# Kernel tuning notes

Measured on AMD Instinct MI355X. Metric: run time of the kernel, lower is better.

## Reference

```python
import jax, jax.numpy as jnp
import numpy as np

N = 100000
E = 1600000
F_NODE = 6
F_EDGE = 2
H = 64


def _glorot(key, shape):
    lim = float(np.sqrt(6.0 / (shape[0] + shape[1])))
    return jax.random.uniform(key, shape, jnp.float32, -lim, lim)


def setup_inputs() -> dict:
    key = jax.random.key(0)
    ks = jax.random.split(key, 16)
    inp = {
        "x": jax.random.normal(ks[0], (N, F_NODE), jnp.float32),
        "edge_index": jax.random.randint(ks[1], (2, E), 0, N, jnp.int64),
        "edge_attr": jax.random.normal(ks[2], (E, F_EDGE), jnp.float32),
        # GCN layers (PyG GCNConv: linear no-bias, then aggregate, then +bias)
        "W1": _glorot(ks[3], (F_NODE, H)), "b1": jnp.zeros((H,), jnp.float32),
        "W2": _glorot(ks[4], (H, H)), "b2": jnp.zeros((H,), jnp.float32),
        "W3": _glorot(ks[5], (H, H)), "b3": jnp.zeros((H,), jnp.float32),
        # edge_mlp
        "We1": _glorot(ks[6], (F_EDGE, H)), "be1": jnp.zeros((H,), jnp.float32),
        "We2": _glorot(ks[7], (H, H)), "be2": jnp.zeros((H,), jnp.float32),
        # predictor
        "Wp1": _glorot(ks[8], (3 * H, H)), "bp1": jnp.zeros((H,), jnp.float32),
        "Wp2": _glorot(ks[9], (H, H // 2)), "bp2": jnp.zeros((H // 2,), jnp.float32),
        "Wp3": _glorot(ks[10], (H // 2, 1)), "bp3": jnp.zeros((1,), jnp.float32),
    }
    return inp


def _gcn_conv(h, W, b, src_sl, dst_sl, norm, n):
    # PyG GCNConv with self-loops and symmetric normalization
    h = h @ W                                   # [N, H_out]
    msg = h[src_sl] * norm[:, None]             # gather + scale per edge(+loop)
    out = jax.ops.segment_sum(msg, dst_sl, num_segments=n)
    return out + b


def _forward(x, edge_attr, W1, b1, W2, b2, W3, b3, We1, be1, We2, be2,
             Wp1, bp1, Wp2, bp2, Wp3, bp3, edge_index):
    n = x.shape[0]
    src, dst = edge_index[0], edge_index[1]

    # --- edge feature injection (vectorized version of per-edge loop) ---
    ef = jax.nn.relu(edge_attr @ We1 + be1) @ We2 + be2      # [E, H]
    nef = (jax.ops.segment_sum(ef, src, num_segments=n)
           + jax.ops.segment_sum(ef, dst, num_segments=n))   # [N, H]
    ones_e = jnp.ones((ef.shape[0],), x.dtype)
    deg = (jax.ops.segment_sum(ones_e, src, num_segments=n)
           + jax.ops.segment_sum(ones_e, dst, num_segments=n))
    deg = jnp.maximum(deg, 1.0)
    nef = nef / deg[:, None]
    # hidden_dim (64) >= node feature dim (6) -> truncate
    x = x + nef[:, : x.shape[1]] * 0.5

    # --- GCN normalization with self-loops (shared across layers) ---
    loop = jnp.arange(n, dtype=src.dtype)
    src_sl = jnp.concatenate([src, loop])
    dst_sl = jnp.concatenate([dst, loop])
    deg_sl = jax.ops.segment_sum(jnp.ones_like(dst_sl, dtype=x.dtype), dst_sl,
                                 num_segments=n)
    dinv = jnp.where(deg_sl > 0, deg_sl ** -0.5, 0.0)
    norm = dinv[src_sl] * dinv[dst_sl]

    h = jax.nn.relu(_gcn_conv(x, W1, b1, src_sl, dst_sl, norm, n))
    h = jax.nn.relu(_gcn_conv(h, W2, b2, src_sl, dst_sl, norm, n))
    h = _gcn_conv(h, W3, b3, src_sl, dst_sl, norm, n)

    graph_emb = h.mean(axis=0)                 # global_mean_pool, batch=None
    node_mean = h.mean(axis=0)
    node_std = jnp.std(h, axis=0, ddof=1)      # torch.std is unbiased
    combined = jnp.concatenate([graph_emb, node_mean, node_std])  # [3H]

    p = jax.nn.relu(combined @ Wp1 + bp1)      # dropout inactive in eval
    p = jax.nn.relu(p @ Wp2 + bp2)
    out = jax.nn.sigmoid(p @ Wp3 + bp3)        # (1,)
    return out


def reference(x, edge_index, edge_attr, W1, b1, W2, b2, W3, b3,
              We1, be1, We2, be2, Wp1, bp1, Wp2, bp2, Wp3, bp3):
    return _forward(x, edge_attr, W1, b1, W2, b2, W3, b3, We1, be1, We2, be2,
                    Wp1, bp1, Wp2, bp2, Wp3, bp3, edge_index)
```

## Files before the change

kernel.cpp:

```cpp
#include <hip/hip_runtime.h>
#include <hip/hip_bf16.h>
#include <stdint.h>

typedef float floatx2 __attribute__((ext_vector_type(2)));

__device__ __forceinline__ float rdlane(float v, int l) {
    return __uint_as_float(__builtin_amdgcn_readlane(__float_as_uint(v), l));
}
__device__ __forceinline__ float bf2f(unsigned short u) {
    return __uint_as_float(((unsigned)u) << 16);
}
__device__ __forceinline__ unsigned short f2bf(float f) {
    unsigned u = __float_as_uint(f);
    u += 0x7fffu + ((u >> 16) & 1u);
    return (unsigned short)(u >> 16);
}
__device__ __forceinline__ unsigned packbf(float a, float b) {
    return (unsigned)f2bf(a) | ((unsigned)f2bf(b) << 16);
}
__device__ __forceinline__ unsigned pk_fp8x4(float a, float b, float c, float d) {
    int u = __builtin_amdgcn_cvt_pk_fp8_f32(a, b, 0, false);
    u = __builtin_amdgcn_cvt_pk_fp8_f32(c, d, u, true);
    return (unsigned)u;
}

__global__ void k_zero(int* __restrict__ cntO, int* __restrict__ cntI,
                       double* __restrict__ sums, int n) {
    int i = blockIdx.x * blockDim.x + threadIdx.x;
    if (i < 128) sums[i] = 0.0;
    if (i < n) { cntO[i] = 0; cntI[i] = 0; }
}

__global__ __launch_bounds__(256) void k_front(
    const int* __restrict__ ei, const float* __restrict__ ea,
    const float* __restrict__ We1, const float* __restrict__ be1,
    const float* __restrict__ We2, const float* __restrict__ be2,
    unsigned* __restrict__ efp, int* __restrict__ cntO, int* __restrict__ cntI,
    int* __restrict__ rankS, int* __restrict__ rankD, int E) {
    __shared__ float sWe1[128], sbe1[64], sWe2[64 * 6], sbe2[6];
    int t = threadIdx.x;
    if (t < 128) sWe1[t] = We1[t];
    if (t < 64) {
        sbe1[t] = be1[t];
#pragma unroll
        for (int c = 0; c < 6; ++c) sWe2[t * 6 + c] = We2[t * 64 + c];
    }
    if (t < 6) sbe2[t] = be2[t];
    __syncthreads();

    int e = blockIdx.x * blockDim.x + t;
    if (e >= E) return;

    int s = ei[e], d = ei[E + e];
    int rs = atomicAdd(&cntO[s], 1);
    int rd = atomicAdd(&cntI[d], 1);

    float2 aa = ((const float2*)ea)[e];
    float a0 = aa.x, a1 = aa.y;
    float acc[6];
#pragma unroll
    for (int c = 0; c < 6; ++c) acc[c] = sbe2[c];
#pragma unroll
    for (int j = 0; j < 64; ++j) {
        float h = fmaf(a0, sWe1[j], fmaf(a1, sWe1[64 + j], sbe1[j]));
        h = fmaxf(h, 0.f);
#pragma unroll
        for (int c = 0; c < 6; ++c) acc[c] = fmaf(h, sWe2[j * 6 + c], acc[c]);
    }
    unsigned* q = efp + (size_t)e * 3;
    q[0] = packbf(acc[0], acc[1]);
    q[1] = packbf(acc[2], acc[3]);
    q[2] = packbf(acc[4], acc[5]);
    rankS[e] = rs;
    rankD[e] = rd;
}

__global__ __launch_bounds__(256) void k_scan1(const int* __restrict__ cntO,
                                               const int* __restrict__ cntI,
                                               int2* __restrict__ bsum, int n) {
    __shared__ int2 l[256];
    int i = blockIdx.x * 256 + threadIdx.x;
    l[threadIdx.x] = (i < n) ? make_int2(cntO[i], cntI[i]) : make_int2(0, 0);
    __syncthreads();
    for (int s = 128; s > 0; s >>= 1) {
        if (threadIdx.x < s) {
            l[threadIdx.x].x += l[threadIdx.x + s].x;
            l[threadIdx.x].y += l[threadIdx.x + s].y;
        }
        __syncthreads();
    }
    if (threadIdx.x == 0) bsum[blockIdx.x] = l[0];
}

__global__ __launch_bounds__(512) void k_scan2(int2* __restrict__ bsum, int nb,
                                               int* __restrict__ offON,
                                               int* __restrict__ offIN) {
    __shared__ int2 l[512];
    int t = threadIdx.x;
    int2 v = (t < nb) ? bsum[t] : make_int2(0, 0);
    l[t] = v;
    __syncthreads();
    for (int s = 1; s < 512; s <<= 1) {
        int2 tmp = (t >= s) ? l[t - s] : make_int2(0, 0);
        __syncthreads();
        l[t].x += tmp.x; l[t].y += tmp.y;
        __syncthreads();
    }
    if (t < nb) bsum[t] = make_int2(l[t].x - v.x, l[t].y - v.y);
    if (t == 511) { *offON = l[511].x; *offIN = l[511].y; }
}

__global__ __launch_bounds__(256) void k_scan3off(const int* __restrict__ cntO,
                                                  const int* __restrict__ cntI,
                                                  const int2* __restrict__ bsum,
                                                  int* __restrict__ offO,
                                                  int* __restrict__ offI, int n) {
    __shared__ int2 l[256];
    int i = blockIdx.x * 256 + threadIdx.x;
    int2 v = (i < n) ? make_int2(cntO[i], cntI[i]) : make_int2(0, 0);
    l[threadIdx.x] = v;
    __syncthreads();
    for (int s = 1; s < 256; s <<= 1) {
        int2 tmp = (threadIdx.x >= (unsigned)s) ? l[threadIdx.x - s] : make_int2(0, 0);
        __syncthreads();
        l[threadIdx.x].x += tmp.x; l[threadIdx.x].y += tmp.y;
        __syncthreads();
    }
    if (i < n) {
        int2 bs = bsum[blockIdx.x];
        offO[i] = l[threadIdx.x].x - v.x + bs.x;
        offI[i] = l[threadIdx.x].y - v.y + bs.y;
    }
}

__global__ __launch_bounds__(256) void k_place(const int* __restrict__ ei,
                                               const int* __restrict__ rankS,
                                               const int* __restrict__ rankD,
                                               const int* __restrict__ offO,
                                               const int* __restrict__ offI,
                                               const unsigned* __restrict__ efp,
                                               unsigned* __restrict__ out_rec,
                                               uint4* __restrict__ in_rec, int E) {
    int e = blockIdx.x * blockDim.x + threadIdx.x;
    if (e >= E) return;
    int s = ei[e], d = ei[E + e];
    const unsigned* q = efp + (size_t)e * 3;
    unsigned u0 = q[0], u1 = q[1], u2 = q[2];
    size_t so = (size_t)(offO[s] + rankS[e]) * 3;
    out_rec[so] = u0; out_rec[so + 1] = u1; out_rec[so + 2] = u2;
    in_rec[offI[d] + rankD[e]] = make_uint4((unsigned)s, u0, u1, u2);
}

__global__ __launch_bounds__(256) void k_nef_x(
    const int* __restrict__ offO, const unsigned* __restrict__ out_rec,
    const int* __restrict__ offI, const uint4* __restrict__ in_rec,
    const float* __restrict__ x,
    float* __restrict__ xp, float* __restrict__ dinv, int n) {
    int i = blockIdx.x * blockDim.x + threadIdx.x;
    if (i >= n) return;
    int bo = offO[i], eo = offO[i + 1];
    int bi = offI[i], eiN = offI[i + 1];
    float a0 = 0.f, a1 = 0.f, a2 = 0.f, a3 = 0.f, a4 = 0.f, a5 = 0.f;
    for (int j = bo; j < eo; ++j) {
        const unsigned* q = out_rec + (size_t)j * 3;
        unsigned u0 = q[0], u1 = q[1], u2 = q[2];
        a0 += bf2f((unsigned short)u0); a1 += bf2f((unsigned short)(u0 >> 16));
        a2 += bf2f((unsigned short)u1); a3 += bf2f((unsigned short)(u1 >> 16));
        a4 += bf2f((unsigned short)u2); a5 += bf2f((unsigned short)(u2 >> 16));
    }
    for (int j = bi; j < eiN; ++j) {
        uint4 r = in_rec[j];
        a0 += bf2f((unsigned short)r.y); a1 += bf2f((unsigned short)(r.y >> 16));
        a2 += bf2f((unsigned short)r.z); a3 += bf2f((unsigned short)(r.z >> 16));
        a4 += bf2f((unsigned short)r.w); a5 += bf2f((unsigned short)(r.w >> 16));
    }
    int indeg = eiN - bi;
    float degf = (float)((eo - bo) + indeg);
    float inv = 0.5f / fmaxf(degf, 1.f);
    xp[(size_t)i * 6 + 0] = x[(size_t)i * 6 + 0] + a0 * inv;
    xp[(size_t)i * 6 + 1] = x[(size_t)i * 6 + 1] + a1 * inv;
    xp[(size_t)i * 6 + 2] = x[(size_t)i * 6 + 2] + a2 * inv;
    xp[(size_t)i * 6 + 3] = x[(size_t)i * 6 + 3] + a3 * inv;
    xp[(size_t)i * 6 + 4] = x[(size_t)i * 6 + 4] + a4 * inv;
    xp[(size_t)i * 6 + 5] = x[(size_t)i * 6 + 5] + a5 * inv;
    dinv[i] = 1.f / sqrtf(1.f + (float)indeg);
}

__global__ __launch_bounds__(256) void k_mm1(const float* __restrict__ xp,
                                             const float* __restrict__ W1,
                                             const float* __restrict__ dinv,
                                             unsigned* __restrict__ sOut, int n) {
    int lane = threadIdx.x & 63;
    int sub = lane & 15;
    int wid = (blockIdx.x * blockDim.x + threadIdx.x) >> 6;
    int nw = (gridDim.x * blockDim.x) >> 6;
    float w[6];
#pragma unroll
    for (int c = 0; c < 6; ++c) w[c] = W1[c * 64 + lane];
    for (int i = wid; i < n; i += nw) {
        float xv = (lane < 6) ? xp[(size_t)i * 6 + lane] : 0.f;
        float acc = 0.f;
#pragma unroll
        for (int c = 0; c < 6; ++c) acc = fmaf(rdlane(xv, c), w[c], acc);
        float o = acc * dinv[i];
        float o0 = __shfl(o, sub * 4 + 0);
        float o1 = __shfl(o, sub * 4 + 1);
        float o2 = __shfl(o, sub * 4 + 2);
        float o3 = __shfl(o, sub * 4 + 3);
        if (lane < 16) sOut[(size_t)i * 16 + lane] = pk_fp8x4(o0, o1, o2, o3);
    }
}

__global__ __launch_bounds__(256) void k_gathermm(
    const int* __restrict__ offI, const uint4* __restrict__ in_rec,
    const float* __restrict__ dinv, const unsigned* __restrict__ sIn,
    const float* __restrict__ bias, const float* __restrict__ W,
    unsigned* __restrict__ sOut, int n) {
    int lane = threadIdx.x & 63;
    int sub = lane & 15, grp = lane >> 4;
    int wid = (blockIdx.x * blockDim.x + threadIdx.x) >> 6;
    int nw = (gridDim.x * blockDim.x) >> 6;
    float w[64];
#pragma unroll
    for (int c = 0; c < 64; ++c) w[c] = W[c * 64 + lane];
    float4 bb = ((const float4*)bias)[sub];

    for (int i = wid; i < n; i += nw) {
        unsigned su = sIn[(size_t)i * 16 + sub];
        float a0, a1, a2, a3;
        if (grp == 0) {
            floatx2 lo = __builtin_amdgcn_cvt_pk_f32_fp8(su, false);
            floatx2 hi = __builtin_amdgcn_cvt_pk_f32_fp8(su, true);
            a0 = lo.x; a1 = lo.y; a2 = hi.x; a3 = hi.y;
        } else { a0 = a1 = a2 = a3 = 0.f; }
        int b0 = offI[i], e0 = offI[i + 1];
#pragma unroll 4
        for (int j = b0 + grp; j < e0; j += 4) {
            unsigned src = in_rec[j].x;
            unsigned u = sIn[(size_t)src * 16 + sub];
            floatx2 lo = __builtin_amdgcn_cvt_pk_f32_fp8(u, false);
            floatx2 hi = __builtin_amdgcn_cvt_pk_f32_fp8(u, true);
            a0 += lo.x; a1 += lo.y; a2 += hi.x; a3 += hi.y;
        }
        a0 += __shfl_xor(a0, 16); a1 += __shfl_xor(a1, 16);
        a2 += __shfl_xor(a2, 16); a3 += __shfl_xor(a3, 16);
        a0 += __shfl_xor(a0, 32); a1 += __shfl_xor(a1, 32);
        a2 += __shfl_xor(a2, 32); a3 += __shfl_xor(a3, 32);

        float dv = dinv[i];
        float h0 = fmaxf(fmaf(a0, dv, bb.x), 0.f);
        float h1 = fmaxf(fmaf(a1, dv, bb.y), 0.f);
        float h2 = fmaxf(fmaf(a2, dv, bb.z), 0.f);
        float h3 = fmaxf(fmaf(a3, dv, bb.w), 0.f);
        float o = 0.f;
#pragma unroll
        for (int g = 0; g < 16; ++g) {
            o = fmaf(rdlane(h0, g), w[g * 4 + 0], o);
            o = fmaf(rdlane(h1, g), w[g * 4 + 1], o);
            o = fmaf(rdlane(h2, g), w[g * 4 + 2], o);
            o = fmaf(rdlane(h3, g), w[g * 4 + 3], o);
        }
        o *= dv;
        float o0 = __shfl(o, sub * 4 + 0);
        float o1 = __shfl(o, sub * 4 + 1);
        float o2 = __shfl(o, sub * 4 + 2);
        float o3 = __shfl(o, sub * 4 + 3);
        if (lane < 16) sOut[(size_t)i * 16 + lane] = pk_fp8x4(o0, o1, o2, o3);
    }
}

__global__ __launch_bounds__(256) void k_gatherreduce(
    const int* __restrict__ offI, const uint4* __restrict__ in_rec,
    const float* __restrict__ dinv, const unsigned* __restrict__ sIn,
    const float* __restrict__ b3, double* __restrict__ sums, int n) {
    int lane = threadIdx.x & 63;
    int sub = lane & 15, grp = lane >> 4;
    int wv = threadIdx.x >> 6;
    int wid = (blockIdx.x * blockDim.x + threadIdx.x) >> 6;
    int nw = (gridDim.x * blockDim.x) >> 6;
    float4 bb = ((const float4*)b3)[sub];
    double s0 = 0.0, s1 = 0.0, s2_ = 0.0, s3 = 0.0;
    double q0 = 0.0, q1 = 0.0, q2 = 0.0, q3 = 0.0;

    for (int i = wid; i < n; i += nw) {
        unsigned su = sIn[(size_t)i * 16 + sub];
        float a0, a1, a2, a3;
        if (grp == 0) {
            floatx2 lo = __builtin_amdgcn_cvt_pk_f32_fp8(su, false);
            floatx2 hi = __builtin_amdgcn_cvt_pk_f32_fp8(su, true);
            a0 = lo.x; a1 = lo.y; a2 = hi.x; a3 = hi.y;
        } else { a0 = a1 = a2 = a3 = 0.f; }
        int b0 = offI[i], e0 = offI[i + 1];
#pragma unroll 4
        for (int j = b0 + grp; j < e0; j += 4) {
            unsigned src = in_rec[j].x;
            unsigned u = sIn[(size_t)src * 16 + sub];
            floatx2 lo = __builtin_amdgcn_cvt_pk_f32_fp8(u, false);
            floatx2 hi = __builtin_amdgcn_cvt_pk_f32_fp8(u, true);
            a0 += lo.x; a1 += lo.y; a2 += hi.x; a3 += hi.y;
        }
        a0 += __shfl_xor(a0, 16); a1 += __shfl_xor(a1, 16);
        a2 += __shfl_xor(a2, 16); a3 += __shfl_xor(a3, 16);
        a0 += __shfl_xor(a0, 32); a1 += __shfl_xor(a1, 32);
        a2 += __shfl_xor(a2, 32); a3 += __shfl_xor(a3, 32);

        float dv = dinv[i];
        float v0 = fmaf(a0, dv, bb.x);
        float v1 = fmaf(a1, dv, bb.y);
        float v2 = fmaf(a2, dv, bb.z);
        float v3 = fmaf(a3, dv, bb.w);
        s0 += v0; s1 += v1; s2_ += v2; s3 += v3;
        q0 += (double)v0 * v0; q1 += (double)v1 * v1;
        q2 += (double)v2 * v2; q3 += (double)v3 * v3;
    }
    __shared__ double shS[4 * 64], shQ[4 * 64];
    if (grp == 0) {
#pragma unroll
        for (int k = 0; k < 4; ++k) {
            double sk = (k == 0) ? s0 : (k == 1) ? s1 : (k == 2) ? s2_ : s3;
            double qk = (k == 0) ? q0 : (k == 1) ? q1 : (k == 2) ? q2 : q3;
            shS[wv * 64 + sub * 4 + k] = sk;
            shQ[wv * 64 + sub * 4 + k] = qk;
        }
    }
    __syncthreads();
    if (wv == 0) {
        double a = shS[lane] + shS[64 + lane] + shS[128 + lane] + shS[192 + lane];
        double c = shQ[lane] + shQ[64 + lane] + shQ[128 + lane] + shQ[192 + lane];
        unsafeAtomicAdd(&sums[lane], a);
        unsafeAtomicAdd(&sums[64 + lane], c);
    }
}

__global__ void k_head(const double* __restrict__ sums,
                       const float* __restrict__ Wp1, const float* __restrict__ bp1,
                       const float* __restrict__ Wp2, const float* __restrict__ bp2,
                       const float* __restrict__ Wp3, const float* __restrict__ bp3,
                       float* __restrict__ out, int n) {
    __shared__ float comb[192], p1[64], p2[32];
    int t = threadIdx.x;
    if (t < 64) {
        double s = sums[t], s2 = sums[64 + t];
        double m = s / n;
        double var = (s2 - s * s / n) / (double)(n - 1);
        float mf = (float)m;
        float sd = (float)sqrt(var > 0.0 ? var : 0.0);
        comb[t] = mf;
        comb[64 + t] = mf;
        comb[128 + t] = sd;
    }
    __syncthreads();
    if (t < 64) {
        float acc = bp1[t];
        for (int k = 0; k < 192; ++k) acc = fmaf(comb[k], Wp1[k * 64 + t], acc);
        p1[t] = fmaxf(acc, 0.f);
    }
    __syncthreads();
    if (t < 32) {
        float acc = bp2[t];
        for (int k = 0; k < 64; ++k) acc = fmaf(p1[k], Wp2[k * 32 + t], acc);
        p2[t] = fmaxf(acc, 0.f);
    }
    __syncthreads();
    if (t == 0) {
        float acc = bp3[0];
        for (int k = 0; k < 32; ++k) acc = fmaf(p2[k], Wp3[k], acc);
        out[0] = 1.f / (1.f + expf(-acc));
    }
}

static inline char* align16(char* p) {
    return (char*)(((uintptr_t)p + 15) & ~(uintptr_t)15);
}

extern "C" void kernel_launch(void* const* d_in, const int* in_sizes, int n_in,
                              void* d_out, int out_size, void* d_ws, size_t ws_size,
                              hipStream_t stream) {
    const float* x   = (const float*)d_in[0];
    const int*   ei  = (const int*)d_in[1];
    const float* ea  = (const float*)d_in[2];
    const float* W1  = (const float*)d_in[3];
    const float* b1  = (const float*)d_in[4];
    const float* W2  = (const float*)d_in[5];
    const float* b2  = (const float*)d_in[6];
    const float* W3  = (const float*)d_in[7];
    const float* b3  = (const float*)d_in[8];
    const float* We1 = (const float*)d_in[9];
    const float* be1 = (const float*)d_in[10];
    const float* We2 = (const float*)d_in[11];
    const float* be2 = (const float*)d_in[12];
    const float* Wp1 = (const float*)d_in[13];
    const float* bp1 = (const float*)d_in[14];
    const float* Wp2 = (const float*)d_in[15];
    const float* bp2 = (const float*)d_in[16];
    const float* Wp3 = (const float*)d_in[17];
    const float* bp3 = (const float*)d_in[18];

    const int N = in_sizes[0] / 6;
    const int E = in_sizes[1] / 2;
    const int nbN = (N + 255) / 256;
    const int nbE = (E + 255) / 256;
    const size_t SB = (size_t)N * 64;

    char* p = (char*)d_ws;
    double* sums = (double*)p;          p = align16(p + 128 * sizeof(double));
    int* cntO = (int*)p;                p = align16(p + (size_t)N * 4);
    int* cntI = (int*)p;                p = align16(p + (size_t)N * 4);
    int* offO = (int*)p;                p = align16(p + ((size_t)N + 1) * 4);
    int* offI = (int*)p;                p = align16(p + ((size_t)N + 1) * 4);
    int2* bsum = (int2*)p;              p = align16(p + 512 * 8);
    float* xp = (float*)p;              p = align16(p + (size_t)N * 6 * 4);
    float* dinv = (float*)p;            p = align16(p + (size_t)N * 4);
    uint4* in_rec = (uint4*)p;          p = align16(p + (size_t)E * 16);
    char* u1 = p;                       p = align16(p + 2 * ((SB + 15) & ~(size_t)15));
    int* rankS = (int*)u1;
    int* rankD = (int*)(u1 + ((SB + 15) & ~(size_t)15));
    unsigned* sbufA = (unsigned*)rankS;
    unsigned* sbufB = (unsigned*)rankD;
    char* u2 = p;
    unsigned* efp = (unsigned*)u2;
    unsigned* out_rec = (unsigned*)(u2 + (size_t)E * 12);

    const int TB = 256;
    dim3 blk(TB);

    k_zero<<<dim3(nbN), blk, 0, stream>>>(cntO, cntI, sums, N);
    k_front<<<dim3(nbE), blk, 0, stream>>>(ei, ea, We1, be1, We2, be2,
                                           efp, cntO, cntI, rankS, rankD, E);
    k_scan1<<<dim3(nbN), blk, 0, stream>>>(cntO, cntI, bsum, N);
    k_scan2<<<dim3(1), dim3(512), 0, stream>>>(bsum, nbN, offO + N, offI + N);
    k_scan3off<<<dim3(nbN), blk, 0, stream>>>(cntO, cntI, bsum, offO, offI, N);
    k_place<<<dim3(nbE), blk, 0, stream>>>(ei, rankS, rankD, offO, offI, efp,
                                           out_rec, in_rec, E);
    k_nef_x<<<dim3(nbN), blk, 0, stream>>>(offO, out_rec, offI, in_rec, x, xp, dinv, N);

    k_mm1<<<dim3(1024), blk, 0, stream>>>(xp, W1, dinv, sbufA, N);
    k_gathermm<<<dim3(2048), blk, 0, stream>>>(offI, in_rec, dinv, sbufA, b1, W2, sbufB, N);
    k_gathermm<<<dim3(2048), blk, 0, stream>>>(offI, in_rec, dinv, sbufB, b2, W3, sbufA, N);
    k_gatherreduce<<<dim3(2048), blk, 0, stream>>>(offI, in_rec, dinv, sbufA, b3, sums, N);
    k_head<<<dim3(1), dim3(64), 0, stream>>>(sums, Wp1, bp1, Wp2, bp2, Wp3, bp3,
                                             (float*)d_out, N);
}
```

Before: 543.8 us.

## Split fp8 node features into halves, compact edge records, fuse mm1

Each 64-wide fp8 node feature buffer is split into two 32-byte halves (lo/hi), and each GCN layer's gather runs as two passes. The intent is a smaller random-gather working set per pass, so it stays resident in L2/MALL. Edge features drop from bf16 to fp8 (8-byte records), and source indices move into a dense int array for the gather loops. The node-edge-feature and first linear layer are fused into one kernel. The cost is extra kernel launches, an fp32 intermediate agg buffer, and more fp8 quantisation error in the edge features.

```diff
diff --git a/kernel.cpp b/kernel.cpp
--- a/kernel.cpp
+++ b/kernel.cpp
@@ -3,25 +3,19 @@
 #include <stdint.h>
 
 typedef float floatx2 __attribute__((ext_vector_type(2)));
+typedef unsigned uint32x4 __attribute__((ext_vector_type(4)));
+typedef float f32x4 __attribute__((ext_vector_type(4)));
 
 __device__ __forceinline__ float rdlane(float v, int l) {
     return __uint_as_float(__builtin_amdgcn_readlane(__float_as_uint(v), l));
-}
-__device__ __forceinline__ float bf2f(unsigned short u) {
-    return __uint_as_float(((unsigned)u) << 16);
-}
-__device__ __forceinline__ unsigned short f2bf(float f) {
-    unsigned u = __float_as_uint(f);
-    u += 0x7fffu + ((u >> 16) & 1u);
-    return (unsigned short)(u >> 16);
-}
-__device__ __forceinline__ unsigned packbf(float a, float b) {
-    return (unsigned)f2bf(a) | ((unsigned)f2bf(b) << 16);
 }
 __device__ __forceinline__ unsigned pk_fp8x4(float a, float b, float c, float d) {
     int u = __builtin_amdgcn_cvt_pk_fp8_f32(a, b, 0, false);
     u = __builtin_amdgcn_cvt_pk_fp8_f32(c, d, u, true);
     return (unsigned)u;
+}
+__device__ __forceinline__ unsigned pk_fp8x2(float a, float b) {
+    return (unsigned)__builtin_amdgcn_cvt_pk_fp8_f32(a, b, 0, false);
 }
 
 __global__ void k_zero(int* __restrict__ cntO, int* __restrict__ cntI,
@@ -35,7 +29,7 @@
     const int* __restrict__ ei, const float* __restrict__ ea,
     const float* __restrict__ We1, const float* __restrict__ be1,
     const float* __restrict__ We2, const float* __restrict__ be2,
-    unsigned* __restrict__ efp, int* __restrict__ cntO, int* __restrict__ cntI,
+    uint2* __restrict__ efp, int* __restrict__ cntO, int* __restrict__ cntI,
     int* __restrict__ rankS, int* __restrict__ rankD, int E) {
     __shared__ float sWe1[128], sbe1[64], sWe2[64 * 6], sbe2[6];
     int t = threadIdx.x;
@@ -56,21 +50,18 @@
     int rd = atomicAdd(&cntI[d], 1);
 
     float2 aa = ((const float2*)ea)[e];
-    float a0 = aa.x, a1 = aa.y;
     float acc[6];
 #pragma unroll
     for (int c = 0; c < 6; ++c) acc[c] = sbe2[c];
 #pragma unroll
     for (int j = 0; j < 64; ++j) {
-        float h = fmaf(a0, sWe1[j], fmaf(a1, sWe1[64 + j], sbe1[j]));
+        float h = fmaf(aa.x, sWe1[j], fmaf(aa.y, sWe1[64 + j], sbe1[j]));
         h = fmaxf(h, 0.f);
 #pragma unroll
         for (int c = 0; c < 6; ++c) acc[c] = fmaf(h, sWe2[j * 6 + c], acc[c]);
     }
-    unsigned* q = efp + (size_t)e * 3;
-    q[0] = packbf(acc[0], acc[1]);
-    q[1] = packbf(acc[2], acc[3]);
-    q[2] = packbf(acc[4], acc[5]);
+    efp[e] = make_uint2(pk_fp8x4(acc[0], acc[1], acc[2], acc[3]),
+                        pk_fp8x2(acc[4], acc[5]));
     rankS[e] = rs;
     rankD[e] = rd;
 }
@@ -91,7 +82,6 @@
     }
     if (threadIdx.x == 0) bsum[blockIdx.x] = l[0];
 }
-
 __global__ __launch_bounds__(512) void k_scan2(int2* __restrict__ bsum, int nb,
                                                int* __restrict__ offON,
                                                int* __restrict__ offIN) {
@@ -109,7 +99,6 @@
     if (t < nb) bsum[t] = make_int2(l[t].x - v.x, l[t].y - v.y);
     if (t == 511) { *offON = l[511].x; *offIN = l[511].y; }
 }
-
 __global__ __launch_bounds__(256) void k_scan3off(const int* __restrict__ cntO,
                                                   const int* __restrict__ cntI,
                                                   const int2* __restrict__ bsum,
@@ -138,95 +127,109 @@
                                                const int* __restrict__ rankD,
                                                const int* __restrict__ offO,
                                                const int* __restrict__ offI,
-                                               const unsigned* __restrict__ efp,
-                                               unsigned* __restrict__ out_rec,
+                                               const uint2* __restrict__ efp,
+                                               uint2* __restrict__ out_rec,
                                                uint4* __restrict__ in_rec, int E) {
     int e = blockIdx.x * blockDim.x + threadIdx.x;
     if (e >= E) return;
     int s = ei[e], d = ei[E + e];
-    const unsigned* q = efp + (size_t)e * 3;
-    unsigned u0 = q[0], u1 = q[1], u2 = q[2];
-    size_t so = (size_t)(offO[s] + rankS[e]) * 3;
-    out_rec[so] = u0; out_rec[so + 1] = u1; out_rec[so + 2] = u2;
-    in_rec[offI[d] + rankD[e]] = make_uint4((unsigned)s, u0, u1, u2);
-}
-
-__global__ __launch_bounds__(256) void k_nef_x(
-    const int* __restrict__ offO, const unsigned* __restrict__ out_rec,
+    uint2 f = efp[e];
+    out_rec[offO[s] + rankS[e]] = f;
+    in_rec[offI[d] + rankD[e]] = make_uint4((unsigned)s, f.x, f.y, 0u);
+}
+
+__global__ __launch_bounds__(256) void k_nefmm1(
+    const int* __restrict__ offO, const uint2* __restrict__ out_rec,
     const int* __restrict__ offI, const uint4* __restrict__ in_rec,
-    const float* __restrict__ x,
-    float* __restrict__ xp, float* __restrict__ dinv, int n) {
-    int i = blockIdx.x * blockDim.x + threadIdx.x;
+    const float* __restrict__ x, const float* __restrict__ W1,
+    float* __restrict__ dinv, int* __restrict__ in_src,
+    unsigned* __restrict__ sLo, unsigned* __restrict__ sHi, int n) {
+    __shared__ float sW1[384];
+    int t = threadIdx.x;
+    for (int idx = t; idx < 384; idx += 256) sW1[idx] = W1[idx];
+    __syncthreads();
+
+    int i = blockIdx.x * blockDim.x + t;
     if (i >= n) return;
     int bo = offO[i], eo = offO[i + 1];
     int bi = offI[i], eiN = offI[i + 1];
     float a0 = 0.f, a1 = 0.f, a2 = 0.f, a3 = 0.f, a4 = 0.f, a5 = 0.f;
     for (int j = bo; j < eo; ++j) {
-        const unsigned* q = out_rec + (size_t)j * 3;
-        unsigned u0 = q[0], u1 = q[1], u2 = q[2];
-        a0 += bf2f((unsigned short)u0); a1 += bf2f((unsigned short)(u0 >> 16));
-        a2 += bf2f((unsigned short)u1); a3 += bf2f((unsigned short)(u1 >> 16));
-        a4 += bf2f((unsigned short)u2); a5 += bf2f((unsigned short)(u2 >> 16));
+        uint2 q = out_rec[j];
+        floatx2 p01 = __builtin_amdgcn_cvt_pk_f32_fp8(q.x, false);
+        floatx2 p23 = __builtin_amdgcn_cvt_pk_f32_fp8(q.x, true);
+        floatx2 p45 = __builtin_amdgcn_cvt_pk_f32_fp8(q.y, false);
+        a0 += p01.x; a1 += p01.y; a2 += p23.x;
+        a3 += p23.y; a4 += p45.x; a5 += p45.y;
     }
     for (int j = bi; j < eiN; ++j) {
         uint4 r = in_rec[j];
-        a0 += bf2f((unsigned short)r.y); a1 += bf2f((unsigned short)(r.y >> 16));
-        a2 += bf2f((unsigned short)r.z); a3 += bf2f((unsigned short)(r.z >> 16));
-        a4 += bf2f((unsigned short)r.w); a5 += bf2f((unsigned short)(r.w >> 16));
+        __builtin_nontemporal_store((int)r.x, in_src + j);
+        floatx2 p01 = __builtin_amdgcn_cvt_pk_f32_fp8(r.y, false);
+        floatx2 p23 = __builtin_amdgcn_cvt_pk_f32_fp8(r.y, true);
+        floatx2 p45 = __builtin_amdgcn_cvt_pk_f32_fp8(r.z, false);
+        a0 += p01.x; a1 += p01.y; a2 += p23.x;
+        a3 += p23.y; a4 += p45.x; a5 += p45.y;
     }
     int indeg = eiN - bi;
     float degf = (float)((eo - bo) + indeg);
     float inv = 0.5f / fmaxf(degf, 1.f);
-    xp[(size_t)i * 6 + 0] = x[(size_t)i * 6 + 0] + a0 * inv;
-    xp[(size_t)i * 6 + 1] = x[(size_t)i * 6 + 1] + a1 * inv;
-    xp[(size_t)i * 6 + 2] = x[(size_t)i * 6 + 2] + a2 * inv;
-    xp[(size_t)i * 6 + 3] = x[(size_t)i * 6 + 3] + a3 * inv;
-    xp[(size_t)i * 6 + 4] = x[(size_t)i * 6 + 4] + a4 * inv;
-    xp[(size_t)i * 6 + 5] = x[(size_t)i * 6 + 5] + a5 * inv;
-    dinv[i] = 1.f / sqrtf(1.f + (float)indeg);
-}
-
-__global__ __launch_bounds__(256) void k_mm1(const float* __restrict__ xp,
-                                             const float* __restrict__ W1,
-                                             const float* __restrict__ dinv,
-                                             unsigned* __restrict__ sOut, int n) {
+    const float2* xr = (const float2*)(x + (size_t)i * 6);
+    float2 x01 = xr[0], x23 = xr[1], x45 = xr[2];
+    float xp0 = x01.x + a0 * inv, xp1 = x01.y + a1 * inv;
+    float xp2 = x23.x + a2 * inv, xp3 = x23.y + a3 * inv;
+    float xp4 = x45.x + a4 * inv, xp5 = x45.y + a5 * inv;
+    float dv = 1.f / sqrtf(1.f + (float)indeg);
+    dinv[i] = dv;
+
+    unsigned u[8];
+#pragma unroll
+    for (int c4 = 0; c4 < 8; ++c4) {
+        float tv[4];
+#pragma unroll
+        for (int k = 0; k < 4; ++k) {
+            int c = c4 * 4 + k;
+            float v = xp0 * sW1[c] + xp1 * sW1[64 + c] + xp2 * sW1[128 + c]
+                    + xp3 * sW1[192 + c] + xp4 * sW1[256 + c] + xp5 * sW1[320 + c];
+            tv[k] = v * dv;
+        }
+        u[c4] = pk_fp8x4(tv[0], tv[1], tv[2], tv[3]);
+    }
+    {
+        uint32x4 v0 = {u[0], u[1], u[2], u[3]};
+        uint32x4 v1 = {u[4], u[5], u[6], u[7]};
+        __builtin_nontemporal_store(v0, (uint32x4*)(sLo + (size_t)i * 8));
+        __builtin_nontemporal_store(v1, (uint32x4*)(sLo + (size_t)i * 8) + 1);
+    }
+#pragma unroll
+    for (int c4 = 0; c4 < 8; ++c4) {
+        float tv[4];
+#pragma unroll
+        for (int k = 0; k < 4; ++k) {
+            int c = 32 + c4 * 4 + k;
+            float v = xp0 * sW1[c] + xp1 * sW1[64 + c] + xp2 * sW1[128 + c]
+                    + xp3 * sW1[192 + c] + xp4 * sW1[256 + c] + xp5 * sW1[320 + c];
+            tv[k] = v * dv;
+        }
+        u[c4] = pk_fp8x4(tv[0], tv[1], tv[2], tv[3]);
+    }
+    {
+        uint32x4 v0 = {u[0], u[1], u[2], u[3]};
+        uint32x4 v1 = {u[4], u[5], u[6], u[7]};
+        __builtin_nontemporal_store(v0, (uint32x4*)(sHi + (size_t)i * 8));
+        __builtin_nontemporal_store(v1, (uint32x4*)(sHi + (size_t)i * 8) + 1);
+    }
+}
+
+__global__ __launch_bounds__(256) void k_gather_lo(
+    const int* __restrict__ offI, const int* __restrict__ in_src,
+    const unsigned* __restrict__ sLo, float* __restrict__ agg, int n) {
     int lane = threadIdx.x & 63;
-    int sub = lane & 15;
+    int sub = lane & 7, grp = lane >> 3;
     int wid = (blockIdx.x * blockDim.x + threadIdx.x) >> 6;
     int nw = (gridDim.x * blockDim.x) >> 6;
-    float w[6];
-#pragma unroll
-    for (int c = 0; c < 6; ++c) w[c] = W1[c * 64 + lane];
     for (int i = wid; i < n; i += nw) {
-        float xv = (lane < 6) ? xp[(size_t)i * 6 + lane] : 0.f;
-        float acc = 0.f;
-#pragma unroll
-        for (int c = 0; c < 6; ++c) acc = fmaf(rdlane(xv, c), w[c], acc);
-        float o = acc * dinv[i];
-        float o0 = __shfl(o, sub * 4 + 0);
-        float o1 = __shfl(o, sub * 4 + 1);
-        float o2 = __shfl(o, sub * 4 + 2);
-        float o3 = __shfl(o, sub * 4 + 3);
-        if (lane < 16) sOut[(size_t)i * 16 + lane] = pk_fp8x4(o0, o1, o2, o3);
-    }
-}
-
-__global__ __launch_bounds__(256) void k_gathermm(
-    const int* __restrict__ offI, const uint4* __restrict__ in_rec,
-    const float* __restrict__ dinv, const unsigned* __restrict__ sIn,
-    const float* __restrict__ bias, const float* __restrict__ W,
-    unsigned* __restrict__ sOut, int n) {
-    int lane = threadIdx.x & 63;
-    int sub = lane & 15, grp = lane >> 4;
-    int wid = (blockIdx.x * blockDim.x + threadIdx.x) >> 6;
-    int nw = (gridDim.x * blockDim.x) >> 6;
-    float w[64];
-#pragma unroll
-    for (int c = 0; c < 64; ++c) w[c] = W[c * 64 + lane];
-    float4 bb = ((const float4*)bias)[sub];
-
-    for (int i = wid; i < n; i += nw) {
-        unsigned su = sIn[(size_t)i * 16 + sub];
+        unsigned su = sLo[(size_t)i * 8 + sub];
         float a0, a1, a2, a3;
         if (grp == 0) {
             floatx2 lo = __builtin_amdgcn_cvt_pk_f32_fp8(su, false);
@@ -235,55 +238,44 @@
         } else { a0 = a1 = a2 = a3 = 0.f; }
         int b0 = offI[i], e0 = offI[i + 1];
 #pragma unroll 4
-        for (int j = b0 + grp; j < e0; j += 4) {
-            unsigned src = in_rec[j].x;
-            unsigned u = sIn[(size_t)src * 16 + sub];
+        for (int j = b0 + grp; j < e0; j += 8) {
+            unsigned src = (unsigned)__builtin_nontemporal_load(in_src + j);
+            unsigned u = sLo[(size_t)src * 8 + sub];
             floatx2 lo = __builtin_amdgcn_cvt_pk_f32_fp8(u, false);
             floatx2 hi = __builtin_amdgcn_cvt_pk_f32_fp8(u, true);
             a0 += lo.x; a1 += lo.y; a2 += hi.x; a3 += hi.y;
         }
+        a0 += __shfl_xor(a0, 8);  a1 += __shfl_xor(a1, 8);
+        a2 += __shfl_xor(a2, 8);  a3 += __shfl_xor(a3, 8);
         a0 += __shfl_xor(a0, 16); a1 += __shfl_xor(a1, 16);
         a2 += __shfl_xor(a2, 16); a3 += __shfl_xor(a3, 16);
         a0 += __shfl_xor(a0, 32); a1 += __shfl_xor(a1, 32);
         a2 += __shfl_xor(a2, 32); a3 += __shfl_xor(a3, 32);
-
-        float dv = dinv[i];
-        float h0 = fmaxf(fmaf(a0, dv, bb.x), 0.f);
-        float h1 = fmaxf(fmaf(a1, dv, bb.y), 0.f);
-        float h2 = fmaxf(fmaf(a2, dv, bb.z), 0.f);
-        float h3 = fmaxf(fmaf(a3, dv, bb.w), 0.f);
-        float o = 0.f;
-#pragma unroll
-        for (int g = 0; g < 16; ++g) {
-            o = fmaf(rdlane(h0, g), w[g * 4 + 0], o);
-            o = fmaf(rdlane(h1, g), w[g * 4 + 1], o);
-            o = fmaf(rdlane(h2, g), w[g * 4 + 2], o);
-            o = fmaf(rdlane(h3, g), w[g * 4 + 3], o);
-        }
-        o *= dv;
-        float o0 = __shfl(o, sub * 4 + 0);
-        float o1 = __shfl(o, sub * 4 + 1);
-        float o2 = __shfl(o, sub * 4 + 2);
-        float o3 = __shfl(o, sub * 4 + 3);
-        if (lane < 16) sOut[(size_t)i * 16 + lane] = pk_fp8x4(o0, o1, o2, o3);
-    }
-}
-
-__global__ __launch_bounds__(256) void k_gatherreduce(
-    const int* __restrict__ offI, const uint4* __restrict__ in_rec,
-    const float* __restrict__ dinv, const unsigned* __restrict__ sIn,
-    const float* __restrict__ b3, double* __restrict__ sums, int n) {
+        if (lane < 8) {
+            f32x4 v = {a0, a1, a2, a3};
+            __builtin_nontemporal_store(v, (f32x4*)(agg + (size_t)i * 32) + lane);
+        }
+    }
+}
+
+__global__ __launch_bounds__(256) void k_gathermm_hi(
+    const int* __restrict__ offI, const int* __restrict__ in_src,
+    const float* __restrict__ dinv, const unsigned* __restrict__ sHiIn,
+    const float* __restrict__ agg, const float* __restrict__ bias,
+    const float* __restrict__ W,
+    unsigned* __restrict__ sLoOut, unsigned* __restrict__ sHiOut, int n) {
     int lane = threadIdx.x & 63;
-    int sub = lane & 15, grp = lane >> 4;
-    int wv = threadIdx.x >> 6;
+    int sub = lane & 7, grp = lane >> 3;
     int wid = (blockIdx.x * blockDim.x + threadIdx.x) >> 6;
     int nw = (gridDim.x * blockDim.x) >> 6;
-    float4 bb = ((const float4*)b3)[sub];
-    double s0 = 0.0, s1 = 0.0, s2_ = 0.0, s3 = 0.0;
-    double q0 = 0.0, q1 = 0.0, q2 = 0.0, q3 = 0.0;
+    float w[64];
+#pragma unroll
+    for (int c = 0; c < 64; ++c) w[c] = W[c * 64 + lane];
+    float blo = bias[lane & 31];
+    float4 bh = ((const float4*)bias)[8 + sub];
 
     for (int i = wid; i < n; i += nw) {
-        unsigned su = sIn[(size_t)i * 16 + sub];
+        unsigned su = sHiIn[(size_t)i * 8 + sub];
         float a0, a1, a2, a3;
         if (grp == 0) {
             floatx2 lo = __builtin_amdgcn_cvt_pk_f32_fp8(su, false);
@@ -292,36 +284,109 @@
         } else { a0 = a1 = a2 = a3 = 0.f; }
         int b0 = offI[i], e0 = offI[i + 1];
 #pragma unroll 4
-        for (int j = b0 + grp; j < e0; j += 4) {
-            unsigned src = in_rec[j].x;
-            unsigned u = sIn[(size_t)src * 16 + sub];
+        for (int j = b0 + grp; j < e0; j += 8) {
+            unsigned src = (unsigned)__builtin_nontemporal_load(in_src + j);
+            unsigned u = sHiIn[(size_t)src * 8 + sub];
             floatx2 lo = __builtin_amdgcn_cvt_pk_f32_fp8(u, false);
             floatx2 hi = __builtin_amdgcn_cvt_pk_f32_fp8(u, true);
             a0 += lo.x; a1 += lo.y; a2 += hi.x; a3 += hi.y;
         }
+        a0 += __shfl_xor(a0, 8);  a1 += __shfl_xor(a1, 8);
+        a2 += __shfl_xor(a2, 8);  a3 += __shfl_xor(a3, 8);
         a0 += __shfl_xor(a0, 16); a1 += __shfl_xor(a1, 16);
         a2 += __shfl_xor(a2, 16); a3 += __shfl_xor(a3, 16);
         a0 += __shfl_xor(a0, 32); a1 += __shfl_xor(a1, 32);
         a2 += __shfl_xor(a2, 32); a3 += __shfl_xor(a3, 32);
 
+        float alo = __builtin_nontemporal_load(agg + (size_t)i * 32 + (lane & 31));
         float dv = dinv[i];
-        float v0 = fmaf(a0, dv, bb.x);
-        float v1 = fmaf(a1, dv, bb.y);
-        float v2 = fmaf(a2, dv, bb.z);
-        float v3 = fmaf(a3, dv, bb.w);
-        s0 += v0; s1 += v1; s2_ += v2; s3 += v3;
-        q0 += (double)v0 * v0; q1 += (double)v1 * v1;
-        q2 += (double)v2 * v2; q3 += (double)v3 * v3;
+        float hlo = fmaxf(fmaf(alo, dv, blo), 0.f);
+        float h0 = fmaxf(fmaf(a0, dv, bh.x), 0.f);
+        float h1 = fmaxf(fmaf(a1, dv, bh.y), 0.f);
+        float h2 = fmaxf(fmaf(a2, dv, bh.z), 0.f);
+        float h3 = fmaxf(fmaf(a3, dv, bh.w), 0.f);
+        float o = 0.f;
+#pragma unroll
+        for (int f = 0; f < 32; ++f) o = fmaf(rdlane(hlo, f), w[f], o);
+#pragma unroll
+        for (int g = 0; g < 8; ++g) {
+            o = fmaf(rdlane(h0, g), w[32 + g * 4 + 0], o);
+            o = fmaf(rdlane(h1, g), w[32 + g * 4 + 1], o);
+            o = fmaf(rdlane(h2, g), w[32 + g * 4 + 2], o);
+            o = fmaf(rdlane(h3, g), w[32 + g * 4 + 3], o);
+        }
+        o *= dv;
+        int s16 = lane & 15;
+        float o0 = __shfl(o, s16 * 4 + 0);
+        float o1 = __shfl(o, s16 * 4 + 1);
+        float o2 = __shfl(o, s16 * 4 + 2);
+        float o3 = __shfl(o, s16 * 4 + 3);
+        unsigned u = pk_fp8x4(o0, o1, o2, o3);
+        if (lane < 8) __builtin_nontemporal_store(u, sLoOut + (size_t)i * 8 + lane);
+        else if (lane < 16) __builtin_nontemporal_store(u, sHiOut + (size_t)i * 8 + lane - 8);
+    }
+}
+
+__global__ __launch_bounds__(256) void k_gatherreduce_hi(
+    const int* __restrict__ offI, const int* __restrict__ in_src,
+    const float* __restrict__ dinv, const unsigned* __restrict__ sHiIn,
+    const float* __restrict__ agg, const float* __restrict__ b3,
+    double* __restrict__ sums, int n) {
+    int lane = threadIdx.x & 63;
+    int sub = lane & 7, grp = lane >> 3;
+    int wv = threadIdx.x >> 6;
+    int wid = (blockIdx.x * blockDim.x + threadIdx.x) >> 6;
+    int nw = (gridDim.x * blockDim.x) >> 6;
+    float blo = b3[lane & 31];
+    float4 bh = ((const float4*)b3)[8 + sub];
+    double sL = 0.0, qL = 0.0;
+    double sH0 = 0.0, sH1 = 0.0, sH2 = 0.0, sH3 = 0.0;
+    double qH0 = 0.0, qH1 = 0.0, qH2 = 0.0, qH3 = 0.0;
+
+    for (int i = wid; i < n; i += nw) {
+        unsigned su = sHiIn[(size_t)i * 8 + sub];
+        float a0, a1, a2, a3;
+        if (grp == 0) {
+            floatx2 lo = __builtin_amdgcn_cvt_pk_f32_fp8(su, false);
+            floatx2 hi = __builtin_amdgcn_cvt_pk_f32_fp8(su, true);
+            a0 = lo.x; a1 = lo.y; a2 = hi.x; a3 = hi.y;
+        } else { a0 = a1 = a2 = a3 = 0.f; }
+        int b0 = offI[i], e0 = offI[i + 1];
+#pragma unroll 4
+        for (int j = b0 + grp; j < e0; j += 8) {
+            unsigned src = (unsigned)__builtin_nontemporal_load(in_src + j);
+            unsigned u = sHiIn[(size_t)src * 8 + sub];
+            floatx2 lo = __builtin_amdgcn_cvt_pk_f32_fp8(u, false);
+            floatx2 hi = __builtin_amdgcn_cvt_pk_f32_fp8(u, true);
+            a0 += lo.x; a1 += lo.y; a2 += hi.x; a3 += hi.y;
+        }
+        a0 += __shfl_xor(a0, 8);  a1 += __shfl_xor(a1, 8);
+        a2 += __shfl_xor(a2, 8);  a3 += __shfl_xor(a3, 8);
+        a0 += __shfl_xor(a0, 16); a1 += __shfl_xor(a1, 16);
+        a2 += __shfl_xor(a2, 16); a3 += __shfl_xor(a3, 16);
+        a0 += __shfl_xor(a0, 32); a1 += __shfl_xor(a1, 32);
+        a2 += __shfl_xor(a2, 32); a3 += __shfl_xor(a3, 32);
+
+        float alo = __builtin_nontemporal_load(agg + (size_t)i * 32 + (lane & 31));
+        float dv = dinv[i];
+        float vlo = fmaf(alo, dv, blo);
+        float v0 = fmaf(a0, dv, bh.x);
+        float v1 = fmaf(a1, dv, bh.y);
+        float v2 = fmaf(a2, dv, bh.z);
+        float v3 = fmaf(a3, dv, bh.w);
+        sL += vlo; qL += (double)vlo * vlo;
+        sH0 += v0; qH0 += (double)v0 * v0;
+        sH1 += v1; qH1 += (double)v1 * v1;
+        sH2 += v2; qH2 += (double)v2 * v2;
+        sH3 += v3; qH3 += (double)v3 * v3;
     }
     __shared__ double shS[4 * 64], shQ[4 * 64];
-    if (grp == 0) {
-#pragma unroll
-        for (int k = 0; k < 4; ++k) {
-            double sk = (k == 0) ? s0 : (k == 1) ? s1 : (k == 2) ? s2_ : s3;
-            double qk = (k == 0) ? q0 : (k == 1) ? q1 : (k == 2) ? q2 : q3;
-            shS[wv * 64 + sub * 4 + k] = sk;
-            shQ[wv * 64 + sub * 4 + k] = qk;
-        }
+    if (lane < 32) { shS[wv * 64 + lane] = sL; shQ[wv * 64 + lane] = qL; }
+    if (lane < 8) {
+        shS[wv * 64 + 32 + lane * 4 + 0] = sH0; shQ[wv * 64 + 32 + lane * 4 + 0] = qH0;
+        shS[wv * 64 + 32 + lane * 4 + 1] = sH1; shQ[wv * 64 + 32 + lane * 4 + 1] = qH1;
+        shS[wv * 64 + 32 + lane * 4 + 2] = sH2; shQ[wv * 64 + 32 + lane * 4 + 2] = qH2;
+        shS[wv * 64 + 32 + lane * 4 + 3] = sH3; shQ[wv * 64 + 32 + lane * 4 + 3] = qH3;
     }
     __syncthreads();
     if (wv == 0) {
@@ -400,7 +465,7 @@
     const int E = in_sizes[1] / 2;
     const int nbN = (N + 255) / 256;
     const int nbE = (E + 255) / 256;
-    const size_t SB = (size_t)N * 64;
+    const size_t HT = ((size_t)N * 32 + 15) & ~(size_t)15;
 
     char* p = (char*)d_ws;
     double* sums = (double*)p;          p = align16(p + 128 * sizeof(double));
@@ -409,20 +474,22 @@
     int* offO = (int*)p;                p = align16(p + ((size_t)N + 1) * 4);
     int* offI = (int*)p;                p = align16(p + ((size_t)N + 1) * 4);
     int2* bsum = (int2*)p;              p = align16(p + 512 * 8);
-    float* xp = (float*)p;              p = align16(p + (size_t)N * 6 * 4);
     float* dinv = (float*)p;            p = align16(p + (size_t)N * 4);
+    int* in_src = (int*)p;              p = align16(p + (size_t)E * 4);
     uint4* in_rec = (uint4*)p;          p = align16(p + (size_t)E * 16);
-    char* u1 = p;                       p = align16(p + 2 * ((SB + 15) & ~(size_t)15));
+    char* u1 = p;                       p = align16(p + 4 * HT);
     int* rankS = (int*)u1;
-    int* rankD = (int*)(u1 + ((SB + 15) & ~(size_t)15));
-    unsigned* sbufA = (unsigned*)rankS;
-    unsigned* sbufB = (unsigned*)rankD;
+    int* rankD = (int*)(u1 + 2 * HT);
+    unsigned* sA_lo = (unsigned*)u1;
+    unsigned* sA_hi = (unsigned*)(u1 + HT);
+    unsigned* sB_lo = (unsigned*)(u1 + 2 * HT);
+    unsigned* sB_hi = (unsigned*)(u1 + 3 * HT);
     char* u2 = p;
-    unsigned* efp = (unsigned*)u2;
-    unsigned* out_rec = (unsigned*)(u2 + (size_t)E * 12);
-
-    const int TB = 256;
-    dim3 blk(TB);
+    uint2* efp = (uint2*)u2;
+    uint2* out_rec = (uint2*)(u2 + (size_t)E * 8);
+    float* agg = (float*)u2;
+
+    dim3 blk(256);
 
     k_zero<<<dim3(nbN), blk, 0, stream>>>(cntO, cntI, sums, N);
     k_front<<<dim3(nbE), blk, 0, stream>>>(ei, ea, We1, be1, We2, be2,
@@ -432,12 +499,18 @@
     k_scan3off<<<dim3(nbN), blk, 0, stream>>>(cntO, cntI, bsum, offO, offI, N);
     k_place<<<dim3(nbE), blk, 0, stream>>>(ei, rankS, rankD, offO, offI, efp,
                                            out_rec, in_rec, E);
-    k_nef_x<<<dim3(nbN), blk, 0, stream>>>(offO, out_rec, offI, in_rec, x, xp, dinv, N);
-
-    k_mm1<<<dim3(1024), blk, 0, stream>>>(xp, W1, dinv, sbufA, N);
-    k_gathermm<<<dim3(2048), blk, 0, stream>>>(offI, in_rec, dinv, sbufA, b1, W2, sbufB, N);
-    k_gathermm<<<dim3(2048), blk, 0, stream>>>(offI, in_rec, dinv, sbufB, b2, W3, sbufA, N);
-    k_gatherreduce<<<dim3(2048), blk, 0, stream>>>(offI, in_rec, dinv, sbufA, b3, sums, N);
+    k_nefmm1<<<dim3(nbN), blk, 0, stream>>>(offO, out_rec, offI, in_rec, x, W1,
+                                            dinv, in_src, sA_lo, sA_hi, N);
+
+    k_gather_lo<<<dim3(2048), blk, 0, stream>>>(offI, in_src, sA_lo, agg, N);
+    k_gathermm_hi<<<dim3(2048), blk, 0, stream>>>(offI, in_src, dinv, sA_hi, agg,
+                                                  b1, W2, sB_lo, sB_hi, N);
+    k_gather_lo<<<dim3(2048), blk, 0, stream>>>(offI, in_src, sB_lo, agg, N);
+    k_gathermm_hi<<<dim3(2048), blk, 0, stream>>>(offI, in_src, dinv, sB_hi, agg,
+                                                  b2, W3, sA_lo, sA_hi, N);
+    k_gather_lo<<<dim3(2048), blk, 0, stream>>>(offI, in_src, sA_lo, agg, N);
+    k_gatherreduce_hi<<<dim3(2048), blk, 0, stream>>>(offI, in_src, dinv, sA_hi, agg,
+                                                      b3, sums, N);
     k_head<<<dim3(1), dim3(64), 0, stream>>>(sums, Wp1, bp1, Wp2, bp2, Wp3, bp3,
                                              (float*)d_out, N);
 }
```

Measured after the change: 648.7 us. 1.19x slower.
